# Kernel optimization log

Measured on AMD Instinct MI355X. Metric: run time of the kernel, lower is better.

## Reference

```python
import jax, jax.numpy as jnp
import numpy as np

DELTA_VAR = 0.5
DELTA_DIST = 1.5
ALPHA, BETA, GAMMA = 1.0, 1.0, 0.001
EPS = 1e-8


def setup_inputs() -> dict:
    key = jax.random.key(0)
    k1, k2 = jax.random.split(key)
    N, D, C = 4_000_000, 16, 64
    features = jax.random.normal(k1, (N, D), dtype=jnp.float32)
    labels = jax.random.randint(k2, (N,), 0, C)  # every cluster id present w.h.p.
    return {"features": features, "labels": labels, "num_clusters": C}


def _discriminative_loss(features, labels, C):
    # per-cluster counts and means (scatter-mean, replaces the boolean-mask loop)
    ones = jnp.ones(features.shape[0], dtype=features.dtype)
    counts = jax.ops.segment_sum(ones, labels, num_segments=C)            # (C,)
    sums = jax.ops.segment_sum(features, labels, num_segments=C)          # (C, D)
    safe_counts = jnp.maximum(counts, 1.0)
    means = sums / safe_counts[:, None]                                   # (C, D)

    # intra-cluster (variance) loss: mean over clusters of mean hinge^2
    dists = jnp.linalg.norm(features - means[labels] + EPS, axis=1)       # (N,)
    hinge2 = jnp.square(jnp.maximum(dists - DELTA_VAR, 0.0))
    per_cluster = jax.ops.segment_sum(hinge2, labels, num_segments=C) / safe_counts
    var_loss = jnp.mean(per_cluster)

    # inter-cluster (distance) loss over all ordered pairs i != j
    diff = means[:, None, :] - means[None, :, :] + EPS                    # (C, C, D)
    pdist = jnp.linalg.norm(diff, axis=-1)                                # (C, C)
    h = jnp.square(jnp.maximum(2.0 * DELTA_DIST - pdist, 0.0))
    h = h * (1.0 - jnp.eye(C, dtype=h.dtype))
    dist_loss = jnp.sum(h) / float(C * (C - 1))

    # regularization: mean centroid norm
    reg_loss = jnp.mean(jnp.linalg.norm(means + EPS, axis=1))

    total = ALPHA * var_loss + BETA * dist_loss + GAMMA * reg_loss
    return jnp.stack([total, var_loss, dist_loss, reg_loss])  # (4,)


def reference(features, labels, num_clusters):
    return _discriminative_loss(features, labels, num_clusters)
```

## Files before the change

kernel.cpp:

```cpp
#include <hip/hip_runtime.h>
#include <math.h>

#define C 64
#define D 16
#define EPSF 1e-8f
#define DVAR 0.5f
#define DDIST 1.5f
#define FPSCALE 65536.0f
#define INV_FPSCALE (1.0f / 65536.0f)
#define VARSCALE 4294967296.0
#define INV_VARSCALE (1.0 / 4294967296.0)
#define BIAS 524288

#define NB 2048
#define NTHR (NB * 256)
#define SLICE 1088

#define GF0 (NB * SLICE)
#define V0 (GF0 + 1088)

__device__ __forceinline__ unsigned long long pack2(float x, float y) {
    unsigned lo = (unsigned)(__float2int_rn(x * FPSCALE) + BIAS);
    unsigned hi = (unsigned)(__float2int_rn(y * FPSCALE) + BIAS);
    return ((unsigned long long)hi << 32) | (unsigned long long)lo;
}

__global__ __launch_bounds__(256) void k_sums(const float4* __restrict__ f4,
                                              const int* __restrict__ labels, int N,
                                              int* __restrict__ arr) {
    __shared__ unsigned long long s_sum2[C * 9];
    __shared__ unsigned s_cnt[C];
    int t = threadIdx.x;
    int b = blockIdx.x;
    for (int i = t; i < C * 9; i += 256) s_sum2[i] = 0ull;
    if (t < C) s_cnt[t] = 0u;
    __syncthreads();

    int nfull = N >> 8;
    for (int it = b; it < nfull; it += NB) {
        int tile = nfull - 1 - it;
        int p = (tile << 8) + t;
        int c = labels[p] & (C - 1);
        float4 a  = f4[4 * p + 0];
        float4 bb = f4[4 * p + 1];
        float4 cc = f4[4 * p + 2];
        float4 dd = f4[4 * p + 3];
        unsigned long long* row = &s_sum2[c * 9];
        atomicAdd(row + 0, pack2(a.x,  a.y));
        atomicAdd(row + 1, pack2(a.z,  a.w));
        atomicAdd(row + 2, pack2(bb.x, bb.y));
        atomicAdd(row + 3, pack2(bb.z, bb.w));
        atomicAdd(row + 4, pack2(cc.x, cc.y));
        atomicAdd(row + 5, pack2(cc.z, cc.w));
        atomicAdd(row + 6, pack2(dd.x, dd.y));
        atomicAdd(row + 7, pack2(dd.z, dd.w));
        atomicAdd(&s_cnt[c], 1u);
    }
    int tail = N & 255;
    if (tail && b == 0 && t < tail) {
        int p = (nfull << 8) + t;
        int c = labels[p] & (C - 1);
        float4 a  = f4[4 * p + 0];
        float4 bb = f4[4 * p + 1];
        float4 cc = f4[4 * p + 2];
        float4 dd = f4[4 * p + 3];
        unsigned long long* row = &s_sum2[c * 9];
        atomicAdd(row + 0, pack2(a.x,  a.y));
        atomicAdd(row + 1, pack2(a.z,  a.w));
        atomicAdd(row + 2, pack2(bb.x, bb.y));
        atomicAdd(row + 3, pack2(bb.z, bb.w));
        atomicAdd(row + 4, pack2(cc.x, cc.y));
        atomicAdd(row + 5, pack2(cc.z, cc.w));
        atomicAdd(row + 6, pack2(dd.x, dd.y));
        atomicAdd(row + 7, pack2(dd.z, dd.w));
        atomicAdd(&s_cnt[c], 1u);
    }
    __syncthreads();
    for (int i = t; i < SLICE; i += 256) {
        int v;
        if (i < C * D) {
            int c = i >> 4, d = i & 15;
            unsigned long long w = s_sum2[c * 9 + (d >> 1)];
            unsigned half = (d & 1) ? (unsigned)(w >> 32) : (unsigned)w;
            v = (int)(half - (s_cnt[c] << 19));
        } else {
            v = (int)s_cnt[i - C * D];
        }
        arr[b * SLICE + i] = v;
    }
}

__global__ __launch_bounds__(256) void k_reduce(const int* __restrict__ arr,
                                                int* __restrict__ g_final) {
    __shared__ int s[256];
    int o = blockIdx.x;
    int t = threadIdx.x;
    int part = 0;
    #pragma unroll
    for (int j = 0; j < NB / 256; j++)
        part += arr[(t + j * 256) * SLICE + o];
    s[t] = part;
    __syncthreads();
    for (int st = 128; st > 0; st >>= 1) {
        if (t < st) s[t] += s[t + st];
        __syncthreads();
    }
    if (t == 0) g_final[o] = s[0];
}

__device__ __forceinline__ float point_term(const float* __restrict__ s_means,
                                            const float* __restrict__ s_w,
                                            float4 a, float4 bb, float4 cc, float4 dd,
                                            int c) {
    const float* m = &s_means[c * 20];
    float4 m0 = *(const float4*)(m + 0);
    float4 m1 = *(const float4*)(m + 4);
    float4 m2 = *(const float4*)(m + 8);
    float4 m3 = *(const float4*)(m + 12);
    float ss = 0.0f, dx;
    dx = a.x - m0.x + EPSF; ss += dx * dx;
    dx = a.y - m0.y + EPSF; ss += dx * dx;
    dx = a.z - m0.z + EPSF; ss += dx * dx;
    dx = a.w - m0.w + EPSF; ss += dx * dx;
    dx = bb.x - m1.x + EPSF; ss += dx * dx;
    dx = bb.y - m1.y + EPSF; ss += dx * dx;
    dx = bb.z - m1.z + EPSF; ss += dx * dx;
    dx = bb.w - m1.w + EPSF; ss += dx * dx;
    dx = cc.x - m2.x + EPSF; ss += dx * dx;
    dx = cc.y - m2.y + EPSF; ss += dx * dx;
    dx = cc.z - m2.z + EPSF; ss += dx * dx;
    dx = cc.w - m2.w + EPSF; ss += dx * dx;
    dx = dd.x - m3.x + EPSF; ss += dx * dx;
    dx = dd.y - m3.y + EPSF; ss += dx * dx;
    dx = dd.z - m3.z + EPSF; ss += dx * dx;
    dx = dd.w - m3.w + EPSF; ss += dx * dx;
    float h = fmaxf(sqrtf(ss) - DVAR, 0.0f);
    return h * h * s_w[c];
}

__global__ __launch_bounds__(256) void k_hinge(const float4* __restrict__ f4,
                                               const int* __restrict__ labels, int N,
                                               const int* __restrict__ g_final,
                                               unsigned long long* __restrict__ g_var) {
    __shared__ __align__(16) float s_means[C * 20];
    __shared__ float s_w[C];
    __shared__ float s_red[256];
    int t = threadIdx.x;
    int b = blockIdx.x;
    for (int i = t; i < C * D; i += 256) {
        int c = i >> 4, d = i & 15;
        float cnt = fmaxf((float)g_final[C * D + c], 1.0f);
        s_means[c * 20 + d] = (float)g_final[i] * INV_FPSCALE / cnt;
    }
    if (t < C) s_w[t] = 1.0f / (fmaxf((float)g_final[C * D + t], 1.0f) * (float)C);
    __syncthreads();

    int gid = b * 256 + t;
    int rounds = N >> 19;
    int rem = N - (rounds << 19);
    float acc = 0.0f;
    int p = gid;
    for (int r = 0; r + 2 <= rounds; r += 2) {
        int p0 = p, p1 = p + NTHR;
        int c0 = labels[p0] & (C - 1);
        int c1 = labels[p1] & (C - 1);
        float4 a0 = f4[4 * p0 + 0], b0 = f4[4 * p0 + 1],
               e0 = f4[4 * p0 + 2], d0 = f4[4 * p0 + 3];
        float4 a1 = f4[4 * p1 + 0], b1 = f4[4 * p1 + 1],
               e1 = f4[4 * p1 + 2], d1 = f4[4 * p1 + 3];
        acc += point_term(s_means, s_w, a0, b0, e0, d0, c0);
        acc += point_term(s_means, s_w, a1, b1, e1, d1, c1);
        p += 2 * NTHR;
    }
    if (rounds & 1) {
        int c0 = labels[p] & (C - 1);
        float4 a0 = f4[4 * p + 0], b0 = f4[4 * p + 1],
               e0 = f4[4 * p + 2], d0 = f4[4 * p + 3];
        acc += point_term(s_means, s_w, a0, b0, e0, d0, c0);
        p += NTHR;
    }
    if (gid < rem) {
        int c0 = labels[p] & (C - 1);
        float4 a0 = f4[4 * p + 0], b0 = f4[4 * p + 1],
               e0 = f4[4 * p + 2], d0 = f4[4 * p + 3];
        acc += point_term(s_means, s_w, a0, b0, e0, d0, c0);
    }
    s_red[t] = acc;
    __syncthreads();
    for (int s = 128; s > 0; s >>= 1) {
        if (t < s) s_red[t] += s_red[t + s];
        __syncthreads();
    }
    if (t == 0)
        g_var[b] = (unsigned long long)((double)s_red[0] * VARSCALE + 0.5);
}

__global__ __launch_bounds__(256) void k_final(const int* __restrict__ g_final,
                                               const unsigned long long* __restrict__ g_var,
                                               float* __restrict__ out) {
    __shared__ float s_m[C * 17];
    __shared__ float red[256];
    __shared__ unsigned long long red64[256];
    int t = threadIdx.x;
    for (int i = t; i < C * D; i += 256) {
        int c = i >> 4, d = i & 15;
        float cnt = fmaxf((float)g_final[C * D + c], 1.0f);
        s_m[c * 17 + d] = (float)g_final[i] * INV_FPSCALE / cnt;
    }
    unsigned long long vq = 0ull;
    #pragma unroll
    for (int j = 0; j < NB / 256; j++) vq += g_var[t + j * 256];
    red64[t] = vq;
    __syncthreads();
    for (int s = 128; s > 0; s >>= 1) {
        if (t < s) red64[t] += red64[t + s];
        __syncthreads();
    }
    float var_loss = (float)((double)red64[0] * INV_VARSCALE);
    __syncthreads();

    float ds = 0.0f;
    for (int p = t; p < C * C; p += 256) {
        int i = p >> 6, j = p & 63;
        if (i != j) {
            float ss = 0.0f;
            #pragma unroll
            for (int d = 0; d < D; d++) {
                float df = s_m[i * 17 + d] - s_m[j * 17 + d] + EPSF;
                ss += df * df;
            }
            float h = fmaxf(2.0f * DDIST - sqrtf(ss), 0.0f);
            ds += h * h;
        }
    }
    red[t] = ds;
    __syncthreads();
    for (int s = 128; s > 0; s >>= 1) {
        if (t < s) red[t] += red[t + s];
        __syncthreads();
    }
    float dist_loss = red[0] / (float)(C * (C - 1));
    __syncthreads();

    float rg = 0.0f;
    if (t < C) {
        float ss = 0.0f;
        #pragma unroll
        for (int d = 0; d < D; d++) {
            float m = s_m[t * 17 + d] + EPSF;
            ss += m * m;
        }
        rg = sqrtf(ss);
    }
    red[t] = rg;
    __syncthreads();
    for (int s = 128; s > 0; s >>= 1) {
        if (t < s) red[t] += red[t + s];
        __syncthreads();
    }
    float reg_loss = red[0] / (float)C;

    if (t == 0) {
        out[0] = var_loss + dist_loss + 0.001f * reg_loss;
        out[1] = var_loss;
        out[2] = dist_loss;
        out[3] = reg_loss;
    }
}

extern "C" void kernel_launch(void* const* d_in, const int* in_sizes, int n_in,
                              void* d_out, int out_size, void* d_ws, size_t ws_size,
                              hipStream_t stream) {
    const float4* f4 = (const float4*)d_in[0];
    const int* labels = (const int*)d_in[1];
    int N = in_sizes[0] / D;

    int* ws = (int*)d_ws;
    int* arr = ws;
    int* g_final = ws + GF0;
    unsigned long long* g_var = (unsigned long long*)(ws + V0);
    float* out = (float*)d_out;

    hipLaunchKernelGGL(k_sums, dim3(NB), dim3(256), 0, stream, f4, labels, N, arr);
    hipLaunchKernelGGL(k_reduce, dim3(SLICE), dim3(256), 0, stream, arr, g_final);
    hipLaunchKernelGGL(k_hinge, dim3(NB), dim3(256), 0, stream, f4, labels, N, g_final, g_var);
    hipLaunchKernelGGL(k_final, dim3(1), dim3(256), 0, stream, g_final, g_var, out);
}
```

Measured before the change: 420.6 us.

## Compute per-cluster sums via bf16 split MFMA with one-hot label matrices

Replaces the LDS 64-bit packed fixed-point atomics in k_sums with matrix-core segment sums. Each wave builds one-hot bf16 label fragments and multiplies them against the features split into hi/lo bf16 parts using mfma_f32_16x16x32_bf16, accumulating in fp32. The per-block partials are now floats, so k_reduce gets a float path. This removes eight LDS atomics per point, but adds scalar per-element feature loads and a hi/lo bf16 split whose precision only approximates fp32. The result is also no longer deterministic fixed-point.

Result: slower. 467.8 us (+11.2%).

```diff
diff --git a/kernel.cpp b/kernel.cpp
--- a/kernel.cpp
+++ b/kernel.cpp
@@ -6,11 +6,8 @@
 #define EPSF 1e-8f
 #define DVAR 0.5f
 #define DDIST 1.5f
-#define FPSCALE 65536.0f
-#define INV_FPSCALE (1.0f / 65536.0f)
 #define VARSCALE 4294967296.0
 #define INV_VARSCALE (1.0 / 4294967296.0)
-#define BIAS 524288
 
 #define NB 2048
 #define NTHR (NB * 256)
@@ -19,93 +16,110 @@
 #define GF0 (NB * SLICE)
 #define V0 (GF0 + 1088)
 
-__device__ __forceinline__ unsigned long long pack2(float x, float y) {
-    unsigned lo = (unsigned)(__float2int_rn(x * FPSCALE) + BIAS);
-    unsigned hi = (unsigned)(__float2int_rn(y * FPSCALE) + BIAS);
-    return ((unsigned long long)hi << 32) | (unsigned long long)lo;
-}
-
-__global__ __launch_bounds__(256) void k_sums(const float4* __restrict__ f4,
+typedef short short8 __attribute__((ext_vector_type(8)));
+typedef float f32x4 __attribute__((ext_vector_type(4)));
+
+__device__ __forceinline__ unsigned bf16rn(float f) {
+    unsigned u = __float_as_uint(f);
+    return (u + 0x7FFFu + ((u >> 16) & 1u)) >> 16;
+}
+
+__global__ __launch_bounds__(256) void k_sums(const float* __restrict__ feat,
                                               const int* __restrict__ labels, int N,
                                               int* __restrict__ arr) {
-    __shared__ unsigned long long s_sum2[C * 9];
+    __shared__ float s_wsum[4 * 1024];
     __shared__ unsigned s_cnt[C];
-    int t = threadIdx.x;
-    int b = blockIdx.x;
-    for (int i = t; i < C * 9; i += 256) s_sum2[i] = 0ull;
+    int t = threadIdx.x, b = blockIdx.x;
+    int w = t >> 6, lane = t & 63;
+    int g = lane >> 4, r = lane & 15;
     if (t < C) s_cnt[t] = 0u;
     __syncthreads();
 
-    int nfull = N >> 8;
-    for (int it = b; it < nfull; it += NB) {
-        int tile = nfull - 1 - it;
-        int p = (tile << 8) + t;
-        int c = labels[p] & (C - 1);
-        float4 a  = f4[4 * p + 0];
-        float4 bb = f4[4 * p + 1];
-        float4 cc = f4[4 * p + 2];
-        float4 dd = f4[4 * p + 3];
-        unsigned long long* row = &s_sum2[c * 9];
-        atomicAdd(row + 0, pack2(a.x,  a.y));
-        atomicAdd(row + 1, pack2(a.z,  a.w));
-        atomicAdd(row + 2, pack2(bb.x, bb.y));
-        atomicAdd(row + 3, pack2(bb.z, bb.w));
-        atomicAdd(row + 4, pack2(cc.x, cc.y));
-        atomicAdd(row + 5, pack2(cc.z, cc.w));
-        atomicAdd(row + 6, pack2(dd.x, dd.y));
-        atomicAdd(row + 7, pack2(dd.z, dd.w));
-        atomicAdd(&s_cnt[c], 1u);
-    }
-    int tail = N & 255;
-    if (tail && b == 0 && t < tail) {
-        int p = (nfull << 8) + t;
-        int c = labels[p] & (C - 1);
-        float4 a  = f4[4 * p + 0];
-        float4 bb = f4[4 * p + 1];
-        float4 cc = f4[4 * p + 2];
-        float4 dd = f4[4 * p + 3];
-        unsigned long long* row = &s_sum2[c * 9];
-        atomicAdd(row + 0, pack2(a.x,  a.y));
-        atomicAdd(row + 1, pack2(a.z,  a.w));
-        atomicAdd(row + 2, pack2(bb.x, bb.y));
-        atomicAdd(row + 3, pack2(bb.z, bb.w));
-        atomicAdd(row + 4, pack2(cc.x, cc.y));
-        atomicAdd(row + 5, pack2(cc.z, cc.w));
-        atomicAdd(row + 6, pack2(dd.x, dd.y));
-        atomicAdd(row + 7, pack2(dd.z, dd.w));
-        atomicAdd(&s_cnt[c], 1u);
-    }
-    __syncthreads();
-    for (int i = t; i < SLICE; i += 256) {
-        int v;
-        if (i < C * D) {
-            int c = i >> 4, d = i & 15;
-            unsigned long long w = s_sum2[c * 9 + (d >> 1)];
-            unsigned half = (d & 1) ? (unsigned)(w >> 32) : (unsigned)w;
-            v = (int)(half - (s_cnt[c] << 19));
-        } else {
-            v = (int)s_cnt[i - C * D];
-        }
-        arr[b * SLICE + i] = v;
-    }
+    f32x4 acc0 = {0.f, 0.f, 0.f, 0.f}, acc1 = {0.f, 0.f, 0.f, 0.f};
+    f32x4 acc2 = {0.f, 0.f, 0.f, 0.f}, acc3 = {0.f, 0.f, 0.f, 0.f};
+
+    int ntiles = (N + 63) >> 6;
+    for (int it = b; it < ntiles; it += NB) {
+        int tile = ntiles - 1 - it;
+        int p0 = (tile << 6) + (w << 4);
+        if (g == 0) {
+            int pc = p0 + r;
+            if (pc < N) atomicAdd(&s_cnt[labels[pc] & 63], 1u);
+        }
+        short8 bfrag;
+        short8 a0, a1, a2, a3;
+        #pragma unroll
+        for (int tt = 0; tt < 4; tt++) {
+            int pt = p0 + (g << 2) + tt;
+            bool ok = pt < N;
+            int lab = ok ? (labels[pt] & 63) : -1;
+            float f = ok ? feat[pt * 16 + r] : 0.0f;
+            unsigned hb = bf16rn(f);
+            float hf = __uint_as_float(hb << 16);
+            unsigned lb = bf16rn(f - hf);
+            bfrag[2 * tt]     = (short)hb;
+            bfrag[2 * tt + 1] = (short)lb;
+            short e0 = (lab == r)      ? (short)0x3F80 : (short)0;
+            short e1 = (lab == r + 16) ? (short)0x3F80 : (short)0;
+            short e2 = (lab == r + 32) ? (short)0x3F80 : (short)0;
+            short e3 = (lab == r + 48) ? (short)0x3F80 : (short)0;
+            a0[2 * tt] = e0; a0[2 * tt + 1] = e0;
+            a1[2 * tt] = e1; a1[2 * tt + 1] = e1;
+            a2[2 * tt] = e2; a2[2 * tt + 1] = e2;
+            a3[2 * tt] = e3; a3[2 * tt + 1] = e3;
+        }
+        acc0 = __builtin_amdgcn_mfma_f32_16x16x32_bf16(a0, bfrag, acc0, 0, 0, 0);
+        acc1 = __builtin_amdgcn_mfma_f32_16x16x32_bf16(a1, bfrag, acc1, 0, 0, 0);
+        acc2 = __builtin_amdgcn_mfma_f32_16x16x32_bf16(a2, bfrag, acc2, 0, 0, 0);
+        acc3 = __builtin_amdgcn_mfma_f32_16x16x32_bf16(a3, bfrag, acc3, 0, 0, 0);
+    }
+    #pragma unroll
+    for (int reg = 0; reg < 4; reg++) {
+        int row = (g << 2) + reg;
+        s_wsum[w * 1024 + (row     ) * 16 + r] = acc0[reg];
+        s_wsum[w * 1024 + (row + 16) * 16 + r] = acc1[reg];
+        s_wsum[w * 1024 + (row + 32) * 16 + r] = acc2[reg];
+        s_wsum[w * 1024 + (row + 48) * 16 + r] = acc3[reg];
+    }
+    __syncthreads();
+    for (int i = t; i < 1024; i += 256) {
+        float s = s_wsum[i] + s_wsum[1024 + i] + s_wsum[2048 + i] + s_wsum[3072 + i];
+        arr[b * SLICE + i] = __float_as_int(s);
+    }
+    if (t < C) arr[b * SLICE + 1024 + t] = (int)s_cnt[t];
 }
 
 __global__ __launch_bounds__(256) void k_reduce(const int* __restrict__ arr,
                                                 int* __restrict__ g_final) {
-    __shared__ int s[256];
+    __shared__ float sf[256];
+    __shared__ int si[256];
     int o = blockIdx.x;
     int t = threadIdx.x;
-    int part = 0;
-    #pragma unroll
-    for (int j = 0; j < NB / 256; j++)
-        part += arr[(t + j * 256) * SLICE + o];
-    s[t] = part;
-    __syncthreads();
-    for (int st = 128; st > 0; st >>= 1) {
-        if (t < st) s[t] += s[t + st];
-        __syncthreads();
-    }
-    if (t == 0) g_final[o] = s[0];
+    if (o < 1024) {
+        float part = 0.0f;
+        #pragma unroll
+        for (int j = 0; j < NB / 256; j++)
+            part += __int_as_float(arr[(t + j * 256) * SLICE + o]);
+        sf[t] = part;
+        __syncthreads();
+        for (int st = 128; st > 0; st >>= 1) {
+            if (t < st) sf[t] += sf[t + st];
+            __syncthreads();
+        }
+        if (t == 0) g_final[o] = __float_as_int(sf[0]);
+    } else {
+        int part = 0;
+        #pragma unroll
+        for (int j = 0; j < NB / 256; j++)
+            part += arr[(t + j * 256) * SLICE + o];
+        si[t] = part;
+        __syncthreads();
+        for (int st = 128; st > 0; st >>= 1) {
+            if (t < st) si[t] += si[t + st];
+            __syncthreads();
+        }
+        if (t == 0) g_final[o] = si[0];
+    }
 }
 
 __device__ __forceinline__ float point_term(const float* __restrict__ s_means,
@@ -150,7 +164,7 @@
     for (int i = t; i < C * D; i += 256) {
         int c = i >> 4, d = i & 15;
         float cnt = fmaxf((float)g_final[C * D + c], 1.0f);
-        s_means[c * 20 + d] = (float)g_final[i] * INV_FPSCALE / cnt;
+        s_means[c * 20 + d] = __int_as_float(g_final[i]) / cnt;
     }
     if (t < C) s_w[t] = 1.0f / (fmaxf((float)g_final[C * D + t], 1.0f) * (float)C);
     __syncthreads();
@@ -205,7 +219,7 @@
     for (int i = t; i < C * D; i += 256) {
         int c = i >> 4, d = i & 15;
         float cnt = fmaxf((float)g_final[C * D + c], 1.0f);
-        s_m[c * 17 + d] = (float)g_final[i] * INV_FPSCALE / cnt;
+        s_m[c * 17 + d] = __int_as_float(g_final[i]) / cnt;
     }
     unsigned long long vq = 0ull;
     #pragma unroll
@@ -271,7 +285,7 @@
 extern "C" void kernel_launch(void* const* d_in, const int* in_sizes, int n_in,
                               void* d_out, int out_size, void* d_ws, size_t ws_size,
                               hipStream_t stream) {
-    const float4* f4 = (const float4*)d_in[0];
+    const float* features = (const float*)d_in[0];
     const int* labels = (const int*)d_in[1];
     int N = in_sizes[0] / D;
 
@@ -281,8 +295,9 @@
     unsigned long long* g_var = (unsigned long long*)(ws + V0);
     float* out = (float*)d_out;
 
-    hipLaunchKernelGGL(k_sums, dim3(NB), dim3(256), 0, stream, f4, labels, N, arr);
+    hipLaunchKernelGGL(k_sums, dim3(NB), dim3(256), 0, stream, features, labels, N, arr);
     hipLaunchKernelGGL(k_reduce, dim3(SLICE), dim3(256), 0, stream, arr, g_final);
-    hipLaunchKernelGGL(k_hinge, dim3(NB), dim3(256), 0, stream, f4, labels, N, g_final, g_var);
+    hipLaunchKernelGGL(k_hinge, dim3(NB), dim3(256), 0, stream,
+                       (const float4*)features, labels, N, g_final, g_var);
     hipLaunchKernelGGL(k_final, dim3(1), dim3(256), 0, stream, g_final, g_var, out);
 }
```
